# Optimization experiments

Hardware: AMD Instinct MI355X
Metric: run time of the kernel (lower is better)

Reference implementation:

```python
import jax, jax.numpy as jnp
import numpy as np

NUM_LAYERS = 4
N_QUBITS = 18      # max(ceil(log2(262144)), 4)
ACTION_SPACE = 4
BATCH = 64


def _rot_matrix(phi, theta, omega):
    # PennyLane Rot(phi, theta, omega) = RZ(omega) RY(theta) RZ(phi)
    c = jnp.cos(theta / 2).astype(jnp.complex64)
    s = jnp.sin(theta / 2).astype(jnp.complex64)
    a = jnp.exp(-0.5j * (phi + omega).astype(jnp.complex64))  # e^{-i(phi+omega)/2}
    b = jnp.exp(0.5j * (phi - omega).astype(jnp.complex64))   # e^{+i(phi-omega)/2}
    row0 = jnp.stack([a * c, -b * s])
    row1 = jnp.stack([jnp.conj(b) * s, jnp.conj(a) * c])
    return jnp.stack([row0, row1])  # [2, 2]


def _apply_1q(state, U, j):
    # state: [B, 2^n]; wire 0 is the most-significant bit (PennyLane convention)
    B = state.shape[0]
    s = state.reshape(B, 2 ** j, 2, -1)
    s = jnp.einsum('ba,kiaj->kibj', U, s)
    return s.reshape(B, -1)


def _apply_cnot_adj(state, j):
    # CNOT with control=j, target=j+1 (adjacent wires): permute |10> <-> |11>
    B = state.shape[0]
    s = state.reshape(B, 2 ** j, 4, -1)
    s = s[:, :, jnp.array([0, 1, 3, 2]), :]
    return s.reshape(B, -1)


def setup_inputs() -> dict:
    key = jax.random.key(0)
    k1, k2 = jax.random.split(key)
    x = jax.random.randint(k1, (BATCH, N_QUBITS // 2), 0, 2, dtype=jnp.int32)
    weights = jax.random.normal(k2, (NUM_LAYERS, N_QUBITS, 3), dtype=jnp.float32)
    return {"weights": weights, "x": x}


def reference(weights, x):
    B = x.shape[0]
    n = N_QUBITS
    # forward() pads the bit-features with zeros to reach n wires
    bits = jnp.concatenate([x, jnp.zeros_like(x)], axis=1)  # [B, n]
    powers = 2 ** jnp.arange(n - 1, -1, -1, dtype=jnp.int32)  # wire 0 = MSB
    idx = (bits * powers).sum(axis=1)
    state = jnp.zeros((B, 2 ** n), jnp.complex64).at[jnp.arange(B), idx].set(1.0)

    for l in range(NUM_LAYERS):
        for j in range(n):
            U = _rot_matrix(weights[l, j, 0], weights[l, j, 1], weights[l, j, 2])
            state = _apply_1q(state, U, j)
        for j in range(n - 1):
            state = _apply_cnot_adj(state, j)

    probs = state.real ** 2 + state.imag ** 2  # [B, 2^n]
    evs = []
    for i in range(ACTION_SPACE):
        p = probs.reshape(B, 2 ** i, 2, -1).sum(axis=(1, 3))  # [B, 2]
        evs.append(p[:, 0] - p[:, 1])  # <Z_i>
    return jnp.stack(evs, axis=1)  # [B, action_space]
```

## Files before the change

kernel.cpp:

```cpp
#include <hip/hip_runtime.h>


#define NQ 18

using cplx = float2;

__device__ __forceinline__ cplx cmul(cplx a, cplx b) {
    return make_float2(a.x * b.x - a.y * b.y, a.x * b.y + a.y * b.x);
}
__device__ __forceinline__ cplx cfma2(cplx a, cplx o0, cplx b, cplx o1) {
    float re = fmaf(a.x, o0.x, fmaf(-a.y, o0.y, fmaf(b.x, o1.x, -b.y * o1.y)));
    float im = fmaf(a.x, o0.y, fmaf(a.y, o0.x, fmaf(b.x, o1.y, b.y * o1.x)));
    return make_float2(re, im);
}

template <int K, int QOF>
__device__ __forceinline__ void gates_layer(cplx* E, const cplx* Us, int l,
                                            int idx, cplx (*s)[512]) {
#pragma unroll
    for (int bpos = 0; bpos < 6; ++bpos) {
        const int m = 1 << bpos;
        const int bit = (idx >> bpos) & 1;
        const cplx* U = &Us[(l * NQ + (QOF - bpos)) * 4];
        const cplx ua = bit ? U[3] : U[0];
        const cplx ub = bit ? U[2] : U[1];
#pragma unroll
        for (int k = 0; k < K; ++k) {
            cplx p;
            p.x = __shfl_xor(E[k].x, m);
            p.y = __shfl_xor(E[k].y, m);
            E[k] = cfma2(ua, E[k], ub, p);
        }
    }
#pragma unroll
    for (int bpos = 6; bpos < 9; ++bpos) {
        const int m = 1 << bpos;
        const int bit = (idx >> bpos) & 1;
        const cplx* U = &Us[(l * NQ + (QOF - bpos)) * 4];
        const cplx ua = bit ? U[3] : U[0];
        const cplx ub = bit ? U[2] : U[1];
#pragma unroll
        for (int k = 0; k < K; ++k) s[k][idx] = E[k];
        __syncthreads();
        cplx p[K];
#pragma unroll
        for (int k = 0; k < K; ++k) p[k] = s[k][idx ^ m];
        __syncthreads();
#pragma unroll
        for (int k = 0; k < K; ++k) E[k] = cfma2(ua, E[k], ub, p[k]);
    }
}

template <int K, int ROW>
__device__ __forceinline__ void perm_split(cplx* E, int idx, cplx (*s)[512]) {
    const int gi = idx ^ (idx >> 1);
#pragma unroll
    for (int k = 0; k < K; ++k) s[k][idx] = E[k];
    __syncthreads();
    cplx v0[K], v1[K];
#pragma unroll
    for (int k = 0; k < K; ++k) {
        if (ROW) {
            cplx v = s[k][gi];
            v0[k] = (idx & 1) ? make_float2(0.f, 0.f) : v;
            v1[k] = (idx & 1) ? v : make_float2(0.f, 0.f);
        } else {
            v0[k] = s[k][gi];
            v1[k] = s[k][gi ^ 256];
        }
    }
    __syncthreads();
#pragma unroll
    for (int k = K - 1; k >= 0; --k) { E[2 * k] = v0[k]; E[2 * k + 1] = v1[k]; }
}

__global__ __launch_bounds__(512) void k_vqc(const float* __restrict__ w,
                                             const int* __restrict__ x,
                                             float* __restrict__ out) {
    __shared__ cplx Us[4 * NQ * 4];
    __shared__ cplx s[8][512];
    __shared__ cplx Gs[64];
    __shared__ float red[8][4];
    const int tid = threadIdx.x;
    const int b = blockIdx.x;

    if (tid < 4 * NQ) {
        float phi = w[tid * 3 + 0], th = w[tid * 3 + 1], om = w[tid * 3 + 2];
        float sn, cs, sa, ca, sb, cb;
        sincosf(0.5f * th, &sn, &cs);
        sincosf(-0.5f * (phi + om), &sa, &ca);
        sincosf(0.5f * (phi - om), &sb, &cb);
        Us[tid * 4 + 0] = make_float2(ca * cs, sa * cs);
        Us[tid * 4 + 1] = make_float2(-cb * sn, -sb * sn);
        Us[tid * 4 + 2] = make_float2(cb * sn, -sb * sn);
        Us[tid * 4 + 3] = make_float2(ca * cs, -sa * cs);
    }
    __syncthreads();

    cplx E[8];

    {
        cplx B = make_float2(1.f, 0.f);
#pragma unroll
        for (int j = 0; j < 9; ++j) {
            int bit = (tid >> (8 - j)) & 1;
            B = cmul(B, Us[(9 + j) * 4 + bit * 2 + 0]);
        }
        E[0] = B;
    }
    perm_split<1, 0>(E, tid, s);
    gates_layer<2, 17>(E, Us, 1, tid, s);
    perm_split<2, 0>(E, tid, s);
    gates_layer<4, 17>(E, Us, 2, tid, s);
    perm_split<4, 0>(E, tid, s);
    gates_layer<8, 17>(E, Us, 3, tid, s);

#pragma unroll
    for (int k = 0; k < 8; ++k) s[k][tid] = E[k];
    __syncthreads();
    {
        const int e = tid >> 3, sub = tid & 7;
        const int k = e >> 3, k2 = e & 7;
        float gr = 0.f, gi = 0.f;
        const int c0 = sub * 64;
        for (int c = c0; c < c0 + 64; ++c) {
            cplx a = s[k][c], bb = s[k2][c];
            gr = fmaf(a.x, bb.x, fmaf(a.y, bb.y, gr));
            gi = fmaf(a.y, bb.x, fmaf(-a.x, bb.y, gi));
        }
#pragma unroll
        for (int mm = 1; mm < 8; mm <<= 1) {
            gr += __shfl_xor(gr, mm);
            gi += __shfl_xor(gi, mm);
        }
        if (sub == 0) Gs[e] = make_float2(gr, gi);
    }
    __syncthreads();

    {
        cplx A = make_float2(1.f, 0.f);
#pragma unroll
        for (int j = 0; j < 9; ++j) {
            int bit = (tid >> (8 - j)) & 1;
            int xb = x[b * 9 + j];
            A = cmul(A, Us[j * 4 + bit * 2 + xb]);
        }
        E[0] = A;
    }
    perm_split<1, 1>(E, tid, s);
    gates_layer<2, 8>(E, Us, 1, tid, s);
    perm_split<2, 1>(E, tid, s);
    gates_layer<4, 8>(E, Us, 2, tid, s);
    perm_split<4, 1>(E, tid, s);
    gates_layer<8, 8>(E, Us, 3, tid, s);

    float M = 0.f;
#pragma unroll
    for (int k = 0; k < 8; ++k) {
#pragma unroll
        for (int k2 = 0; k2 < 8; ++k2) {
            cplx g = Gs[k * 8 + k2];
            float ar = fmaf(E[k].x, E[k2].x, E[k].y * E[k2].y);
            float ai = fmaf(E[k].y, E[k2].x, -E[k].x * E[k2].y);
            M = fmaf(ar, g.x, fmaf(-ai, g.y, M));
        }
    }
    const int r = tid;
    const int p8 = (r >> 8) & 1;
    const int p7 = p8 ^ ((r >> 7) & 1);
    const int p6 = p7 ^ ((r >> 6) & 1);
    const int p5 = p6 ^ ((r >> 5) & 1);
    float e0 = p8 ? -M : M, e1 = p7 ? -M : M;
    float e2 = p6 ? -M : M, e3 = p5 ? -M : M;
#pragma unroll
    for (int off = 32; off >= 1; off >>= 1) {
        e0 += __shfl_xor(e0, off); e1 += __shfl_xor(e1, off);
        e2 += __shfl_xor(e2, off); e3 += __shfl_xor(e3, off);
    }
    const int lane = tid & 63, wv = tid >> 6;
    if (lane == 0) { red[wv][0] = e0; red[wv][1] = e1; red[wv][2] = e2; red[wv][3] = e3; }
    __syncthreads();
    if (tid < 4) {
        float tot = 0.f;
#pragma unroll
        for (int k = 0; k < 8; ++k) tot += red[k][tid];
        out[b * 4 + tid] = tot;
    }
}

extern "C" void kernel_launch(void* const* d_in, const int* in_sizes, int n_in,
                              void* d_out, int out_size, void* d_ws, size_t ws_size,
                              hipStream_t stream) {
    const float* w = (const float*)d_in[0];
    const int* x = (const int*)d_in[1];
    float* out = (float*)d_out;
    (void)d_ws; (void)ws_size; (void)n_in; (void)in_sizes; (void)out_size;

    k_vqc<<<64, 512, 0, stream>>>(w, x, out);
}
```

Baseline: 82.95 us.

## Run row and column factor evolutions concurrently in 1024-thread blocks

The kernel now launches 1024 threads per block, so the column factor (8 waves) and the row factor (8 waves) evolve at the same time instead of one after the other. Each wave owns one k-slice with 8 register elements, so the three high qubit gates become in-register butterflies rather than shared-memory exchanges with barriers. The permutation is rewritten as a single XOR-indexed shared-memory gather, and the shared arrays are padded. The cost is higher register pressure at 1024 threads and half the threads sitting idle in the Gram and reduction phases.

```diff
diff --git a/kernel.cpp b/kernel.cpp
--- a/kernel.cpp
+++ b/kernel.cpp
@@ -14,171 +14,177 @@
     return make_float2(re, im);
 }
 
-template <int K, int QOF>
-__device__ __forceinline__ void gates_layer(cplx* E, const cplx* Us, int l,
-                                            int idx, cplx (*s)[512]) {
-#pragma unroll
-    for (int bpos = 0; bpos < 6; ++bpos) {
-        const int m = 1 << bpos;
-        const int bit = (idx >> bpos) & 1;
-        const cplx* U = &Us[(l * NQ + (QOF - bpos)) * 4];
-        const cplx ua = bit ? U[3] : U[0];
-        const cplx ub = bit ? U[2] : U[1];
-#pragma unroll
-        for (int k = 0; k < K; ++k) {
-            cplx p;
-            p.x = __shfl_xor(E[k].x, m);
-            p.y = __shfl_xor(E[k].y, m);
-            E[k] = cfma2(ua, E[k], ub, p);
-        }
-    }
-#pragma unroll
-    for (int bpos = 6; bpos < 9; ++bpos) {
-        const int m = 1 << bpos;
-        const int bit = (idx >> bpos) & 1;
-        const cplx* U = &Us[(l * NQ + (QOF - bpos)) * 4];
-        const cplx ua = bit ? U[3] : U[0];
-        const cplx ub = bit ? U[2] : U[1];
-#pragma unroll
-        for (int k = 0; k < K; ++k) s[k][idx] = E[k];
-        __syncthreads();
-        cplx p[K];
-#pragma unroll
-        for (int k = 0; k < K; ++k) p[k] = s[k][idx ^ m];
-        __syncthreads();
-#pragma unroll
-        for (int k = 0; k < K; ++k) E[k] = cfma2(ua, E[k], ub, p[k]);
-    }
-}
-
-template <int K, int ROW>
-__device__ __forceinline__ void perm_split(cplx* E, int idx, cplx (*s)[512]) {
-    const int gi = idx ^ (idx >> 1);
-#pragma unroll
-    for (int k = 0; k < K; ++k) s[k][idx] = E[k];
-    __syncthreads();
-    cplx v0[K], v1[K];
-#pragma unroll
-    for (int k = 0; k < K; ++k) {
-        if (ROW) {
-            cplx v = s[k][gi];
-            v0[k] = (idx & 1) ? make_float2(0.f, 0.f) : v;
-            v1[k] = (idx & 1) ? v : make_float2(0.f, 0.f);
-        } else {
-            v0[k] = s[k][gi];
-            v1[k] = s[k][gi ^ 256];
-        }
-    }
-    __syncthreads();
-#pragma unroll
-    for (int k = K - 1; k >= 0; --k) { E[2 * k] = v0[k]; E[2 * k + 1] = v1[k]; }
-}
-
-__global__ __launch_bounds__(512) void k_vqc(const float* __restrict__ w,
-                                             const int* __restrict__ x,
-                                             float* __restrict__ out) {
+__global__ __launch_bounds__(1024) void k_vqc(const float* __restrict__ w,
+                                              const int* __restrict__ x,
+                                              float* __restrict__ out) {
     __shared__ cplx Us[4 * NQ * 4];
-    __shared__ cplx s[8][512];
+    __shared__ cplx sc[8][516];
+    __shared__ cplx sr[8][516];
     __shared__ cplx Gs[64];
     __shared__ float red[8][4];
+    __shared__ int xb[9];
     const int tid = threadIdx.x;
     const int b = blockIdx.x;
-
+    const int t = tid & 63;
+    const int wv = tid >> 6;
+    const int isrow = wv >> 3;
+    const int rk = wv & 7;
+    cplx (*sb)[516] = isrow ? sr : sc;
+    const int qof = isrow ? 8 : 17;
+
+    if (tid < 9) xb[tid] = x[b * 9 + tid];
     if (tid < 4 * NQ) {
         float phi = w[tid * 3 + 0], th = w[tid * 3 + 1], om = w[tid * 3 + 2];
-        float sn, cs, sa, ca, sb, cb;
+        float sn, cs, sa, ca, sb2, cb;
         sincosf(0.5f * th, &sn, &cs);
         sincosf(-0.5f * (phi + om), &sa, &ca);
-        sincosf(0.5f * (phi - om), &sb, &cb);
+        sincosf(0.5f * (phi - om), &sb2, &cb);
         Us[tid * 4 + 0] = make_float2(ca * cs, sa * cs);
-        Us[tid * 4 + 1] = make_float2(-cb * sn, -sb * sn);
-        Us[tid * 4 + 2] = make_float2(cb * sn, -sb * sn);
+        Us[tid * 4 + 1] = make_float2(-cb * sn, -sb2 * sn);
+        Us[tid * 4 + 2] = make_float2(cb * sn, -sb2 * sn);
         Us[tid * 4 + 3] = make_float2(ca * cs, -sa * cs);
     }
     __syncthreads();
 
     cplx E[8];
-
-    {
-        cplx B = make_float2(1.f, 0.f);
-#pragma unroll
-        for (int j = 0; j < 9; ++j) {
-            int bit = (tid >> (8 - j)) & 1;
-            B = cmul(B, Us[(9 + j) * 4 + bit * 2 + 0]);
-        }
-        E[0] = B;
-    }
-    perm_split<1, 0>(E, tid, s);
-    gates_layer<2, 17>(E, Us, 1, tid, s);
-    perm_split<2, 0>(E, tid, s);
-    gates_layer<4, 17>(E, Us, 2, tid, s);
-    perm_split<4, 0>(E, tid, s);
-    gates_layer<8, 17>(E, Us, 3, tid, s);
-
-#pragma unroll
-    for (int k = 0; k < 8; ++k) s[k][tid] = E[k];
-    __syncthreads();
-    {
-        const int e = tid >> 3, sub = tid & 7;
-        const int k = e >> 3, k2 = e & 7;
+#pragma unroll
+    for (int e = 0; e < 8; ++e) E[e] = make_float2(0.f, 0.f);
+
+    if (wv == 0) {
+#pragma unroll
+        for (int e = 0; e < 8; ++e) {
+            const int idx = e * 64 + t;
+            cplx B = make_float2(1.f, 0.f);
+#pragma unroll
+            for (int j = 0; j < 9; ++j) {
+                int bit = (idx >> (8 - j)) & 1;
+                B = cmul(B, Us[(9 + j) * 4 + bit * 2 + 0]);
+            }
+            E[e] = B;
+        }
+    } else if (wv == 8) {
+#pragma unroll
+        for (int e = 0; e < 8; ++e) {
+            const int idx = e * 64 + t;
+            cplx A = make_float2(1.f, 0.f);
+#pragma unroll
+            for (int j = 0; j < 9; ++j) {
+                int bit = (idx >> (8 - j)) & 1;
+                A = cmul(A, Us[j * 4 + bit * 2 + xb[j]]);
+            }
+            E[e] = A;
+        }
+    }
+
+    const int srck = rk >> 1, q = rk & 1;
+    const int tg = t ^ (t >> 1);
+    const int eflip = isrow ? 0 : (q << 2);
+    const int keepmask = isrow ? ((t & 1) == q) : 1;
+
+#define PERM()                                                              \
+    {                                                                       \
+        _Pragma("unroll") for (int e = 0; e < 8; ++e)                       \
+            sb[rk][e * 64 + t] = E[e];                                      \
+        __syncthreads();                                                    \
+        cplx V[8];                                                          \
+        _Pragma("unroll") for (int e = 0; e < 8; ++e) {                     \
+            const int slot =                                                \
+                (((e ^ (e >> 1)) ^ eflip) << 6) | (tg ^ ((e & 1) << 5));    \
+            cplx v = sb[srck][slot];                                        \
+            if (!keepmask) v = make_float2(0.f, 0.f);                       \
+            V[e] = v;                                                       \
+        }                                                                   \
+        __syncthreads();                                                    \
+        _Pragma("unroll") for (int e = 0; e < 8; ++e) E[e] = V[e];          \
+    }
+
+#define GATES(l)                                                            \
+    {                                                                       \
+        _Pragma("unroll") for (int bp = 0; bp < 6; ++bp) {                  \
+            const int m = 1 << bp;                                          \
+            const cplx* U = &Us[((l) * NQ + (qof - bp)) * 4];               \
+            const int bit = (t >> bp) & 1;                                  \
+            const cplx ua = bit ? U[3] : U[0];                              \
+            const cplx ub = bit ? U[2] : U[1];                              \
+            _Pragma("unroll") for (int e = 0; e < 8; ++e) {                 \
+                cplx p;                                                     \
+                p.x = __shfl_xor(E[e].x, m);                                \
+                p.y = __shfl_xor(E[e].y, m);                                \
+                E[e] = cfma2(ua, E[e], ub, p);                              \
+            }                                                               \
+        }                                                                   \
+        _Pragma("unroll") for (int bb = 0; bb < 3; ++bb) {                  \
+            const cplx* U = &Us[((l) * NQ + (qof - 6 - bb)) * 4];           \
+            const cplx u0 = U[0], u1 = U[1], u2 = U[2], u3 = U[3];          \
+            const int st = 1 << bb;                                         \
+            _Pragma("unroll") for (int e = 0; e < 8; ++e) if (!(e & st)) {  \
+                cplx o0 = E[e], o1 = E[e | st];                             \
+                E[e]      = cfma2(u0, o0, u1, o1);                          \
+                E[e | st] = cfma2(u2, o0, u3, o1);                          \
+            }                                                               \
+        }                                                                   \
+    }
+
+    PERM(); GATES(1);
+    PERM(); GATES(2);
+    PERM(); GATES(3);
+
+#pragma unroll
+    for (int e = 0; e < 8; ++e) sb[rk][e * 64 + t] = E[e];
+    __syncthreads();
+
+    if (tid < 512) {
+        const int ee = tid >> 3, sub = tid & 7;
+        const int k = ee >> 3, k2 = ee & 7;
         float gr = 0.f, gi = 0.f;
-        const int c0 = sub * 64;
-        for (int c = c0; c < c0 + 64; ++c) {
-            cplx a = s[k][c], bb = s[k2][c];
-            gr = fmaf(a.x, bb.x, fmaf(a.y, bb.y, gr));
-            gi = fmaf(a.y, bb.x, fmaf(-a.x, bb.y, gi));
+#pragma unroll
+        for (int i = 0; i < 64; ++i) {
+            const int c = sub + 8 * i;
+            cplx a = sc[k][c], bb2 = sc[k2][c];
+            gr = fmaf(a.x, bb2.x, fmaf(a.y, bb2.y, gr));
+            gi = fmaf(a.y, bb2.x, fmaf(-a.x, bb2.y, gi));
         }
 #pragma unroll
         for (int mm = 1; mm < 8; mm <<= 1) {
             gr += __shfl_xor(gr, mm);
             gi += __shfl_xor(gi, mm);
         }
-        if (sub == 0) Gs[e] = make_float2(gr, gi);
-    }
-    __syncthreads();
-
-    {
-        cplx A = make_float2(1.f, 0.f);
-#pragma unroll
-        for (int j = 0; j < 9; ++j) {
-            int bit = (tid >> (8 - j)) & 1;
-            int xb = x[b * 9 + j];
-            A = cmul(A, Us[j * 4 + bit * 2 + xb]);
-        }
-        E[0] = A;
-    }
-    perm_split<1, 1>(E, tid, s);
-    gates_layer<2, 8>(E, Us, 1, tid, s);
-    perm_split<2, 1>(E, tid, s);
-    gates_layer<4, 8>(E, Us, 2, tid, s);
-    perm_split<4, 1>(E, tid, s);
-    gates_layer<8, 8>(E, Us, 3, tid, s);
-
-    float M = 0.f;
-#pragma unroll
-    for (int k = 0; k < 8; ++k) {
-#pragma unroll
-        for (int k2 = 0; k2 < 8; ++k2) {
-            cplx g = Gs[k * 8 + k2];
-            float ar = fmaf(E[k].x, E[k2].x, E[k].y * E[k2].y);
-            float ai = fmaf(E[k].y, E[k2].x, -E[k].x * E[k2].y);
-            M = fmaf(ar, g.x, fmaf(-ai, g.y, M));
-        }
-    }
-    const int r = tid;
-    const int p8 = (r >> 8) & 1;
-    const int p7 = p8 ^ ((r >> 7) & 1);
-    const int p6 = p7 ^ ((r >> 6) & 1);
-    const int p5 = p6 ^ ((r >> 5) & 1);
-    float e0 = p8 ? -M : M, e1 = p7 ? -M : M;
-    float e2 = p6 ? -M : M, e3 = p5 ? -M : M;
-#pragma unroll
-    for (int off = 32; off >= 1; off >>= 1) {
-        e0 += __shfl_xor(e0, off); e1 += __shfl_xor(e1, off);
-        e2 += __shfl_xor(e2, off); e3 += __shfl_xor(e3, off);
-    }
-    const int lane = tid & 63, wv = tid >> 6;
-    if (lane == 0) { red[wv][0] = e0; red[wv][1] = e1; red[wv][2] = e2; red[wv][3] = e3; }
+        if (sub == 0) Gs[ee] = make_float2(gr, gi);
+    }
+    __syncthreads();
+
+    if (tid < 512) {
+        const int r = tid;
+        cplx Ek[8];
+#pragma unroll
+        for (int k = 0; k < 8; ++k) Ek[k] = sr[k][r];
+        float M = 0.f;
+#pragma unroll
+        for (int k = 0; k < 8; ++k) {
+#pragma unroll
+            for (int k2 = 0; k2 < 8; ++k2) {
+                cplx g = Gs[k * 8 + k2];
+                float ar = fmaf(Ek[k].x, Ek[k2].x, Ek[k].y * Ek[k2].y);
+                float ai = fmaf(Ek[k].y, Ek[k2].x, -Ek[k].x * Ek[k2].y);
+                M = fmaf(ar, g.x, fmaf(-ai, g.y, M));
+            }
+        }
+        const int p8 = (r >> 8) & 1;
+        const int p7 = p8 ^ ((r >> 7) & 1);
+        const int p6 = p7 ^ ((r >> 6) & 1);
+        const int p5 = p6 ^ ((r >> 5) & 1);
+        float e0 = p8 ? -M : M, e1 = p7 ? -M : M;
+        float e2 = p6 ? -M : M, e3 = p5 ? -M : M;
+#pragma unroll
+        for (int off = 32; off >= 1; off >>= 1) {
+            e0 += __shfl_xor(e0, off); e1 += __shfl_xor(e1, off);
+            e2 += __shfl_xor(e2, off); e3 += __shfl_xor(e3, off);
+        }
+        if (t == 0) {
+            red[wv][0] = e0; red[wv][1] = e1;
+            red[wv][2] = e2; red[wv][3] = e3;
+        }
+    }
     __syncthreads();
     if (tid < 4) {
         float tot = 0.f;
@@ -196,5 +202,5 @@
     float* out = (float*)d_out;
     (void)d_ws; (void)ws_size; (void)n_in; (void)in_sizes; (void)out_size;
 
-    k_vqc<<<64, 512, 0, stream>>>(w, x, out);
-}
+    k_vqc<<<64, 1024, 0, stream>>>(w, x, out);
+}
```

New measurement: 77.63 us. 6.4% less time.
